# Kernel tuning notes

Measured on AMD Instinct MI355X. Metric: run time of the kernel, lower is better.

Reference implementation:

```python
import jax, jax.numpy as jnp
import numpy as np

B, D, H, L = 131072, 64, 256, 8  # batch, input_dim, hidden_dim, n_coupling_layers


def _alternating_masks():
    m = np.zeros((L, D), np.float32)
    m[:, ::2] = 1.0            # even layers: mask = 1,0,1,0,...
    m[1::2] = 1.0 - m[1::2]    # odd layers:  mask = 0,1,0,1,...
    return jnp.asarray(m)


def setup_inputs() -> dict:
    key = jax.random.key(0)
    ks = jax.random.split(key, 14)

    def lin_w(k, o, i):
        return (jax.random.normal(k, (L, o, i), jnp.float32) / np.sqrt(i))

    return {
        "x": jax.random.normal(ks[0], (B, D), jnp.float32),
        "masks": _alternating_masks(),                      # [L, D]
        # scale network params (stacked over layers)
        "sW1": lin_w(ks[1], H, D), "sb1": jnp.zeros((L, H), jnp.float32),
        "sW2": lin_w(ks[2], H, H), "sb2": jnp.zeros((L, H), jnp.float32),
        "sW3": lin_w(ks[3], D, H), "sb3": jnp.zeros((L, D), jnp.float32),
        "scale": 0.1 * jax.random.normal(ks[4], (L, D), jnp.float32),
        # translation network params
        "tW1": lin_w(ks[5], H, D), "tb1": jnp.zeros((L, H), jnp.float32),
        "tW2": lin_w(ks[6], H, H), "tb2": jnp.zeros((L, H), jnp.float32),
        "tW3": lin_w(ks[7], D, H), "tb3": jnp.zeros((L, D), jnp.float32),
    }


def _flow(x, masks, sW1, sb1, sW2, sb2, sW3, sb3, scale,
          tW1, tb1, tW2, tb2, tW3, tb3):
    def layer(carry, p):
        y, ld = carry
        m, W1, b1, W2, b2, W3, b3, sc, V1, c1, V2, c2, V3, c3 = p
        xm = y * m                                   # masked input [B, D]
        # scale net: residual tanh MLP, ends with +xm then elementwise *sc
        s = jnp.tanh(xm @ W1.T + b1)
        s = jnp.tanh(s @ W2.T + b2 + s)
        s = (jnp.tanh(s @ W3.T + b3) + xm) * sc
        # translation net
        t = jnp.tanh(xm @ V1.T + c1)
        t = jnp.tanh(t @ V2.T + c2 + t)
        t = (t @ V3.T + c3) + xm
        y2 = m * y + (1.0 - m) * (y * jnp.exp(s) + t)
        ld2 = ld + jnp.sum((1.0 - m) * s, -1)
        return (y2, ld2), None

    init = (x, jnp.zeros(x.shape[0], x.dtype))
    xs = (masks, sW1, sb1, sW2, sb2, sW3, sb3, scale,
          tW1, tb1, tW2, tb2, tW3, tb3)
    (y, logdet), _ = jax.lax.scan(layer, init, xs)
    return y, logdet


def reference(x, masks, sW1, sb1, sW2, sb2, sW3, sb3, scale,
              tW1, tb1, tW2, tb2, tW3, tb3):
    return _flow(x, masks, sW1, sb1, sW2, sb2, sW3, sb3, scale,
                 tW1, tb1, tW2, tb2, tW3, tb3)
```

## Files before the change

### kernel.cpp

```cpp
#include <hip/hip_runtime.h>


#define BATCH    131072
#define DIM      64
#define HID      256
#define NLAYER   8
#define BM       64
#define NTHREADS 256

#define ACT_S 264
#define XM_S  72
#define S3_S  68

typedef _Float16 f16;
typedef __attribute__((ext_vector_type(8))) _Float16 f16x8;
typedef __attribute__((ext_vector_type(4))) _Float16 f16x4;
typedef __attribute__((ext_vector_type(2))) _Float16 f16x2;
typedef __attribute__((ext_vector_type(4))) float    f32x4;

#define TWO_LOG2E 2.8853900817779268f
#define LOG2E     1.4426950408889634f

__device__ __forceinline__ float tanh_fast(float x) {
  float e = __builtin_amdgcn_exp2f(x * TWO_LOG2E);
  return 1.f - 2.f * __builtin_amdgcn_rcpf(e + 1.f);
}

__device__ __forceinline__ f16x4 pk4(float a, float b, float c, float d) {
  f16x2 lo = __builtin_bit_cast(f16x2, __builtin_amdgcn_cvt_pkrtz(a, b));
  f16x2 hi = __builtin_bit_cast(f16x2, __builtin_amdgcn_cvt_pkrtz(c, d));
  f16x4 o; o[0] = lo[0]; o[1] = lo[1]; o[2] = hi[0]; o[3] = hi[1];
  return o;
}

__global__ void cvt6_kernel(const float* s0, f16* d0, const float* s1, f16* d1,
                            const float* s2, f16* d2, const float* s3, f16* d3,
                            const float* s4, f16* d4, const float* s5, f16* d5) {
  int i = blockIdx.x * blockDim.x + threadIdx.x;
  const float* s; f16* d; int base;
  if      (i < 32768)  { s = s0; d = d0; base = 0; }
  else if (i < 163840) { s = s1; d = d1; base = 32768; }
  else if (i < 196608) { s = s2; d = d2; base = 163840; }
  else if (i < 229376) { s = s3; d = d3; base = 196608; }
  else if (i < 360448) { s = s4; d = d4; base = 229376; }
  else                 { s = s5; d = d5; base = 360448; }
  int k = i - base;
  float4 v = ((const float4*)s)[k];
  ((f16x4*)d)[k] = pk4(v.x, v.y, v.z, v.w);
}

__global__ __launch_bounds__(NTHREADS, 3) void flow_kernel(
    const float* __restrict__ x, const float* __restrict__ masks,
    const f16* __restrict__ wS1, const f16* __restrict__ wS2, const f16* __restrict__ wS3,
    const float* __restrict__ sb1, const float* __restrict__ sb2, const float* __restrict__ sb3,
    const float* __restrict__ scl,
    const f16* __restrict__ wT1, const f16* __restrict__ wT2, const f16* __restrict__ wT3,
    const float* __restrict__ tb1, const float* __restrict__ tb2, const float* __restrict__ tb3,
    float* __restrict__ y_out, float* __restrict__ ld_out)
{
  __shared__ __attribute__((aligned(16))) f16 act [BM * ACT_S];
  __shared__ __attribute__((aligned(16))) f16 xm_s[BM * XM_S];
  __shared__ __attribute__((aligned(16))) f16 s3_s[BM * S3_S];
  float* ld_red = (float*)xm_s;
  (void)masks;

  const int tid  = threadIdx.x;
  const int lane = tid & 63;
  const int wv   = tid >> 6;
  const int quad = lane >> 4;
  const int l16  = lane & 15;
  const int row0 = blockIdx.x * BM;
  const int d0   = wv * 16 + quad * 4;

  float yv[4][4];
  float lda[4];
  #pragma unroll
  for (int n = 0; n < 4; ++n) {
    const float4 v = *(const float4*)&x[(size_t)(row0 + n * 16 + l16) * DIM + d0];
    yv[n][0] = v.x; yv[n][1] = v.y; yv[n][2] = v.z; yv[n][3] = v.w;
    lda[n] = 0.f;
  }

  const f32x4 fzero = {0.f, 0.f, 0.f, 0.f};

  #pragma unroll 1
  for (int l = 0; l < NLAYER; ++l) {
    const int par = l & 1;

    if (par == 0) {
      #pragma unroll
      for (int n = 0; n < 4; ++n)
        *(f16x4*)&xm_s[(n * 16 + l16) * XM_S + d0] =
            pk4(yv[n][0], 0.f, yv[n][2], 0.f);
    } else {
      #pragma unroll
      for (int n = 0; n < 4; ++n)
        *(f16x4*)&xm_s[(n * 16 + l16) * XM_S + d0] =
            pk4(0.f, yv[n][1], 0.f, yv[n][3]);
    }
    __syncthreads();

    #pragma unroll 1
    for (int net = 0; net < 2; ++net) {
      const f16*   W1 = (net ? wT1 : wS1) + l * HID * DIM;
      const f16*   W2 = (net ? wT2 : wS2) + l * HID * HID;
      const f16*   W3 = (net ? wT3 : wS3) + l * DIM * HID;
      const float* b1 = (net ? tb1 : sb1) + l * HID;
      const float* b2 = (net ? tb2 : sb2) + l * HID;
      const float* b3 = (net ? tb3 : sb3) + l * DIM;

      f32x4 acc[4][4];
      #pragma unroll
      for (int m = 0; m < 4; ++m)
        #pragma unroll
        for (int n = 0; n < 4; ++n) acc[m][n] = fzero;

      #pragma unroll
      for (int kt = 0; kt < 2; ++kt) {
        const int k0 = kt * 32 + quad * 8;
        f16x8 afr[4];
        #pragma unroll
        for (int m = 0; m < 4; ++m)
          afr[m] = *(const f16x8*)&W1[(wv * 64 + m * 16 + l16) * DIM + k0];
        #pragma unroll
        for (int n = 0; n < 4; ++n) {
          const f16x8 bfr = *(const f16x8*)&xm_s[(n * 16 + l16) * XM_S + k0];
          #pragma unroll
          for (int m = 0; m < 4; ++m)
            acc[m][n] = __builtin_amdgcn_mfma_f32_16x16x32_f16(afr[m], bfr, acc[m][n], 0, 0, 0);
        }
      }
      #pragma unroll
      for (int m = 0; m < 4; ++m) {
        const int   h0  = wv * 64 + m * 16 + quad * 4;
        const float4 bv = *(const float4*)&b1[h0];
        #pragma unroll
        for (int n = 0; n < 4; ++n)
          *(f16x4*)&act[(n * 16 + l16) * ACT_S + h0] =
              pk4(tanh_fast(acc[m][n][0] + bv.x), tanh_fast(acc[m][n][1] + bv.y),
                  tanh_fast(acc[m][n][2] + bv.z), tanh_fast(acc[m][n][3] + bv.w));
      }
      __syncthreads();

      #pragma unroll
      for (int m = 0; m < 4; ++m)
        #pragma unroll
        for (int n = 0; n < 4; ++n) acc[m][n] = fzero;
      #pragma unroll 2
      for (int kt = 0; kt < 8; ++kt) {
        const int k0 = kt * 32 + quad * 8;
        f16x8 afr[4];
        #pragma unroll
        for (int m = 0; m < 4; ++m)
          afr[m] = *(const f16x8*)&W2[(wv * 64 + m * 16 + l16) * HID + k0];
        #pragma unroll
        for (int n = 0; n < 4; ++n) {
          const f16x8 bfr = *(const f16x8*)&act[(n * 16 + l16) * ACT_S + k0];
          #pragma unroll
          for (int m = 0; m < 4; ++m)
            acc[m][n] = __builtin_amdgcn_mfma_f32_16x16x32_f16(afr[m], bfr, acc[m][n], 0, 0, 0);
        }
      }
      __syncthreads();
      #pragma unroll
      for (int m = 0; m < 4; ++m) {
        const int   h0  = wv * 64 + m * 16 + quad * 4;
        const float4 bv = *(const float4*)&b2[h0];
        #pragma unroll
        for (int n = 0; n < 4; ++n) {
          f16x4* p = (f16x4*)&act[(n * 16 + l16) * ACT_S + h0];
          const f16x4 prev = *p;
          *p = pk4(tanh_fast(acc[m][n][0] + bv.x + (float)prev[0]),
                   tanh_fast(acc[m][n][1] + bv.y + (float)prev[1]),
                   tanh_fast(acc[m][n][2] + bv.z + (float)prev[2]),
                   tanh_fast(acc[m][n][3] + bv.w + (float)prev[3]));
        }
      }
      __syncthreads();

      f32x4 acc3[4];
      #pragma unroll
      for (int n = 0; n < 4; ++n) acc3[n] = fzero;
      #pragma unroll 2
      for (int kt = 0; kt < 8; ++kt) {
        const int k0  = kt * 32 + quad * 8;
        const f16x8 a3 = *(const f16x8*)&W3[(wv * 16 + l16) * HID + k0];
        #pragma unroll
        for (int n = 0; n < 4; ++n) {
          const f16x8 bfr = *(const f16x8*)&act[(n * 16 + l16) * ACT_S + k0];
          acc3[n] = __builtin_amdgcn_mfma_f32_16x16x32_f16(a3, bfr, acc3[n], 0, 0, 0);
        }
      }
      if (net == 0) __syncthreads();

      const float4 b3v = *(const float4*)&b3[d0];
      if (net == 0) {
        const float4 sv = *(const float4*)&scl[l * DIM + d0];
        if (par == 0) {
          #pragma unroll
          for (int n = 0; n < 4; ++n)
            *(f16x4*)&s3_s[(n * 16 + l16) * S3_S + d0] =
                pk4(0.f, tanh_fast(acc3[n][1] + b3v.y) * sv.y,
                    0.f, tanh_fast(acc3[n][3] + b3v.w) * sv.w);
        } else {
          #pragma unroll
          for (int n = 0; n < 4; ++n)
            *(f16x4*)&s3_s[(n * 16 + l16) * S3_S + d0] =
                pk4(tanh_fast(acc3[n][0] + b3v.x) * sv.x, 0.f,
                    tanh_fast(acc3[n][2] + b3v.z) * sv.z, 0.f);
        }
      } else {
        #define EP3I(n, r, BC) {                                         \
          const float s = (float)sh[r];                                  \
          const float e = __builtin_amdgcn_exp2f(s * LOG2E);             \
          yv[n][r] = yv[n][r] * e + (acc3[n][r] + (BC));                 \
          lda[n] += s; }
        if (par == 0) {
          #pragma unroll
          for (int n = 0; n < 4; ++n) {
            const f16x4 sh = *(const f16x4*)&s3_s[(n * 16 + l16) * S3_S + d0];
            EP3I(n, 1, b3v.y)
            EP3I(n, 3, b3v.w)
          }
        } else {
          #pragma unroll
          for (int n = 0; n < 4; ++n) {
            const f16x4 sh = *(const f16x4*)&s3_s[(n * 16 + l16) * S3_S + d0];
            EP3I(n, 0, b3v.x)
            EP3I(n, 2, b3v.z)
          }
        }
        #undef EP3I
      }
    }
  }

  #pragma unroll
  for (int n = 0; n < 4; ++n) {
    float4 v; v.x = yv[n][0]; v.y = yv[n][1]; v.z = yv[n][2]; v.w = yv[n][3];
    *(float4*)&y_out[(size_t)(row0 + n * 16 + l16) * DIM + d0] = v;
  }

  float v0 = lda[0], v1 = lda[1], v2 = lda[2], v3 = lda[3];
  v0 += __shfl_xor(v0, 16); v0 += __shfl_xor(v0, 32);
  v1 += __shfl_xor(v1, 16); v1 += __shfl_xor(v1, 32);
  v2 += __shfl_xor(v2, 16); v2 += __shfl_xor(v2, 32);
  v3 += __shfl_xor(v3, 16); v3 += __shfl_xor(v3, 32);
  __syncthreads();
  if (quad == 0) {
    ld_red[(0 * 16 + l16) * 4 + wv] = v0;
    ld_red[(1 * 16 + l16) * 4 + wv] = v1;
    ld_red[(2 * 16 + l16) * 4 + wv] = v2;
    ld_red[(3 * 16 + l16) * 4 + wv] = v3;
  }
  __syncthreads();
  if (tid < BM)
    ld_out[row0 + tid] = ld_red[tid * 4 + 0] + ld_red[tid * 4 + 1]
                       + ld_red[tid * 4 + 2] + ld_red[tid * 4 + 3];
}

extern "C" void kernel_launch(void* const* d_in, const int* in_sizes, int n_in,
                              void* d_out, int out_size, void* d_ws, size_t ws_size,
                              hipStream_t stream) {
  const float* x     = (const float*)d_in[0];
  const float* masks = (const float*)d_in[1];
  const float* sW1f  = (const float*)d_in[2];
  const float* sb1   = (const float*)d_in[3];
  const float* sW2f  = (const float*)d_in[4];
  const float* sb2   = (const float*)d_in[5];
  const float* sW3f  = (const float*)d_in[6];
  const float* sb3   = (const float*)d_in[7];
  const float* scl   = (const float*)d_in[8];
  const float* tW1f  = (const float*)d_in[9];
  const float* tb1   = (const float*)d_in[10];
  const float* tW2f  = (const float*)d_in[11];
  const float* tb2   = (const float*)d_in[12];
  const float* tW3f  = (const float*)d_in[13];
  const float* tb3   = (const float*)d_in[14];
  (void)in_sizes; (void)n_in; (void)out_size; (void)ws_size;

  const int W1SZ = NLAYER * HID * DIM;
  const int W2SZ = NLAYER * HID * HID;
  const int W3SZ = NLAYER * DIM * HID;
  f16* wS1 = (f16*)d_ws;
  f16* wS2 = wS1 + W1SZ;
  f16* wS3 = wS2 + W2SZ;
  f16* wT1 = wS3 + W3SZ;
  f16* wT2 = wT1 + W1SZ;
  f16* wT3 = wT2 + W2SZ;

  cvt6_kernel<<<1536, 256, 0, stream>>>(sW1f, wS1, sW2f, wS2, sW3f, wS3,
                                        tW1f, wT1, tW2f, wT2, tW3f, wT3);

  float* y_out  = (float*)d_out;
  float* ld_out = y_out + (size_t)BATCH * DIM;
  flow_kernel<<<BATCH / BM, NTHREADS, 0, stream>>>(
      x, masks, wS1, wS2, wS3, sb1, sb2, sb3, scl,
      wT1, wT2, wT3, tb1, tb2, tb3, y_out, ld_out);
}
```

Before: 896.7 us.

## Pack masked W1 columns, fold biases into accumulators, keep scale in registers

```diff
diff --git a/kernel.cpp b/kernel.cpp
--- a/kernel.cpp
+++ b/kernel.cpp
@@ -8,9 +8,8 @@
 #define BM       64
 #define NTHREADS 256
 
-#define ACT_S 264
-#define XM_S  72
-#define S3_S  68
+#define ACT_S  264
+#define XMP_S  32
 
 typedef _Float16 f16;
 typedef __attribute__((ext_vector_type(8))) _Float16 f16x8;
@@ -26,42 +25,58 @@
   return 1.f - 2.f * __builtin_amdgcn_rcpf(e + 1.f);
 }
 
+__device__ __forceinline__ f16x2 pk2(float a, float b) {
+  return __builtin_bit_cast(f16x2, __builtin_amdgcn_cvt_pkrtz(a, b));
+}
+
 __device__ __forceinline__ f16x4 pk4(float a, float b, float c, float d) {
-  f16x2 lo = __builtin_bit_cast(f16x2, __builtin_amdgcn_cvt_pkrtz(a, b));
-  f16x2 hi = __builtin_bit_cast(f16x2, __builtin_amdgcn_cvt_pkrtz(c, d));
+  f16x2 lo = pk2(a, b);
+  f16x2 hi = pk2(c, d);
   f16x4 o; o[0] = lo[0]; o[1] = lo[1]; o[2] = hi[0]; o[3] = hi[1];
   return o;
 }
 
-__global__ void cvt6_kernel(const float* s0, f16* d0, const float* s1, f16* d1,
-                            const float* s2, f16* d2, const float* s3, f16* d3,
-                            const float* s4, f16* d4, const float* s5, f16* d5) {
+__global__ void cvt4_kernel(const float* s0, f16* d0, const float* s1, f16* d1,
+                            const float* s2, f16* d2, const float* s3, f16* d3) {
   int i = blockIdx.x * blockDim.x + threadIdx.x;
   const float* s; f16* d; int base;
-  if      (i < 32768)  { s = s0; d = d0; base = 0; }
-  else if (i < 163840) { s = s1; d = d1; base = 32768; }
-  else if (i < 196608) { s = s2; d = d2; base = 163840; }
-  else if (i < 229376) { s = s3; d = d3; base = 196608; }
-  else if (i < 360448) { s = s4; d = d4; base = 229376; }
-  else                 { s = s5; d = d5; base = 360448; }
+  if      (i < 131072) { s = s0; d = d0; base = 0; }
+  else if (i < 163840) { s = s1; d = d1; base = 131072; }
+  else if (i < 294912) { s = s2; d = d2; base = 163840; }
+  else                 { s = s3; d = d3; base = 294912; }
   int k = i - base;
   float4 v = ((const float4*)s)[k];
   ((f16x4*)d)[k] = pk4(v.x, v.y, v.z, v.w);
 }
 
-__global__ __launch_bounds__(NTHREADS, 3) void flow_kernel(
+__global__ void cvtW1p_kernel(const float* sW1f, f16* dS,
+                              const float* tW1f, f16* dT) {
+  int i = blockIdx.x * blockDim.x + threadIdx.x;
+  const float* s = (i < 32768) ? sW1f : tW1f;
+  f16*         d = (i < 32768) ? dS   : dT;
+  int j   = i & 32767;
+  int l   = j >> 12;
+  int rem = j & 4095;
+  int h   = rem >> 4;
+  int kq  = rem & 15;
+  int par = l & 1;
+  const float a = s[l * 16384 + h * 64 + 4 * kq + par];
+  const float b = s[l * 16384 + h * 64 + 4 * kq + 2 + par];
+  ((f16x2*)d)[j] = pk2(a, b);
+}
+
+__global__ __launch_bounds__(NTHREADS, 4) void flow_kernel(
     const float* __restrict__ x, const float* __restrict__ masks,
-    const f16* __restrict__ wS1, const f16* __restrict__ wS2, const f16* __restrict__ wS3,
+    const f16* __restrict__ wS1p, const f16* __restrict__ wS2, const f16* __restrict__ wS3,
     const float* __restrict__ sb1, const float* __restrict__ sb2, const float* __restrict__ sb3,
     const float* __restrict__ scl,
-    const f16* __restrict__ wT1, const f16* __restrict__ wT2, const f16* __restrict__ wT3,
+    const f16* __restrict__ wT1p, const f16* __restrict__ wT2, const f16* __restrict__ wT3,
     const float* __restrict__ tb1, const float* __restrict__ tb2, const float* __restrict__ tb3,
     float* __restrict__ y_out, float* __restrict__ ld_out)
 {
   __shared__ __attribute__((aligned(16))) f16 act [BM * ACT_S];
-  __shared__ __attribute__((aligned(16))) f16 xm_s[BM * XM_S];
-  __shared__ __attribute__((aligned(16))) f16 s3_s[BM * S3_S];
-  float* ld_red = (float*)xm_s;
+  __shared__ __attribute__((aligned(16))) f16 xm_p[BM * XMP_S];
+  float* ld_red = (float*)xm_p;
   (void)masks;
 
   const int tid  = threadIdx.x;
@@ -71,8 +86,10 @@
   const int l16  = lane & 15;
   const int row0 = blockIdx.x * BM;
   const int d0   = wv * 16 + quad * 4;
-
-  float yv[4][4];
+  const int dp   = d0 >> 1;
+
+  float yv [4][4];
+  float s3r[4][2];
   float lda[4];
   #pragma unroll
   for (int n = 0; n < 4; ++n) {
@@ -81,8 +98,6 @@
     lda[n] = 0.f;
   }
 
-  const f32x4 fzero = {0.f, 0.f, 0.f, 0.f};
-
   #pragma unroll 1
   for (int l = 0; l < NLAYER; ++l) {
     const int par = l & 1;
@@ -90,41 +105,40 @@
     if (par == 0) {
       #pragma unroll
       for (int n = 0; n < 4; ++n)
-        *(f16x4*)&xm_s[(n * 16 + l16) * XM_S + d0] =
-            pk4(yv[n][0], 0.f, yv[n][2], 0.f);
+        *(f16x2*)&xm_p[(n * 16 + l16) * XMP_S + dp] = pk2(yv[n][0], yv[n][2]);
     } else {
       #pragma unroll
       for (int n = 0; n < 4; ++n)
-        *(f16x4*)&xm_s[(n * 16 + l16) * XM_S + d0] =
-            pk4(0.f, yv[n][1], 0.f, yv[n][3]);
+        *(f16x2*)&xm_p[(n * 16 + l16) * XMP_S + dp] = pk2(yv[n][1], yv[n][3]);
     }
     __syncthreads();
 
     #pragma unroll 1
     for (int net = 0; net < 2; ++net) {
-      const f16*   W1 = (net ? wT1 : wS1) + l * HID * DIM;
-      const f16*   W2 = (net ? wT2 : wS2) + l * HID * HID;
-      const f16*   W3 = (net ? wT3 : wS3) + l * DIM * HID;
+      const f16*   W1 = (net ? wT1p : wS1p) + l * HID * 32;
+      const f16*   W2 = (net ? wT2  : wS2)  + l * HID * HID;
+      const f16*   W3 = (net ? wT3  : wS3)  + l * DIM * HID;
       const float* b1 = (net ? tb1 : sb1) + l * HID;
       const float* b2 = (net ? tb2 : sb2) + l * HID;
       const float* b3 = (net ? tb3 : sb3) + l * DIM;
 
       f32x4 acc[4][4];
-      #pragma unroll
-      for (int m = 0; m < 4; ++m)
-        #pragma unroll
-        for (int n = 0; n < 4; ++n) acc[m][n] = fzero;
-
-      #pragma unroll
-      for (int kt = 0; kt < 2; ++kt) {
-        const int k0 = kt * 32 + quad * 8;
+
+      #pragma unroll
+      for (int m = 0; m < 4; ++m) {
+        const float4 bv = *(const float4*)&b1[wv * 64 + m * 16 + quad * 4];
+        f32x4 bi; bi[0] = bv.x; bi[1] = bv.y; bi[2] = bv.z; bi[3] = bv.w;
+        #pragma unroll
+        for (int n = 0; n < 4; ++n) acc[m][n] = bi;
+      }
+      {
         f16x8 afr[4];
         #pragma unroll
         for (int m = 0; m < 4; ++m)
-          afr[m] = *(const f16x8*)&W1[(wv * 64 + m * 16 + l16) * DIM + k0];
+          afr[m] = *(const f16x8*)&W1[(wv * 64 + m * 16 + l16) * 32 + quad * 8];
         #pragma unroll
         for (int n = 0; n < 4; ++n) {
-          const f16x8 bfr = *(const f16x8*)&xm_s[(n * 16 + l16) * XM_S + k0];
+          const f16x8 bfr = *(const f16x8*)&xm_p[(n * 16 + l16) * XMP_S + quad * 8];
           #pragma unroll
           for (int m = 0; m < 4; ++m)
             acc[m][n] = __builtin_amdgcn_mfma_f32_16x16x32_f16(afr[m], bfr, acc[m][n], 0, 0, 0);
@@ -132,20 +146,22 @@
       }
       #pragma unroll
       for (int m = 0; m < 4; ++m) {
-        const int   h0  = wv * 64 + m * 16 + quad * 4;
-        const float4 bv = *(const float4*)&b1[h0];
+        const int h0 = wv * 64 + m * 16 + quad * 4;
         #pragma unroll
         for (int n = 0; n < 4; ++n)
           *(f16x4*)&act[(n * 16 + l16) * ACT_S + h0] =
-              pk4(tanh_fast(acc[m][n][0] + bv.x), tanh_fast(acc[m][n][1] + bv.y),
-                  tanh_fast(acc[m][n][2] + bv.z), tanh_fast(acc[m][n][3] + bv.w));
+              pk4(tanh_fast(acc[m][n][0]), tanh_fast(acc[m][n][1]),
+                  tanh_fast(acc[m][n][2]), tanh_fast(acc[m][n][3]));
       }
       __syncthreads();
 
       #pragma unroll
-      for (int m = 0; m < 4; ++m)
-        #pragma unroll
-        for (int n = 0; n < 4; ++n) acc[m][n] = fzero;
+      for (int m = 0; m < 4; ++m) {
+        const float4 bv = *(const float4*)&b2[wv * 64 + m * 16 + quad * 4];
+        f32x4 bi; bi[0] = bv.x; bi[1] = bv.y; bi[2] = bv.z; bi[3] = bv.w;
+        #pragma unroll
+        for (int n = 0; n < 4; ++n) acc[m][n] = bi;
+      }
       #pragma unroll 2
       for (int kt = 0; kt < 8; ++kt) {
         const int k0 = kt * 32 + quad * 8;
@@ -164,23 +180,26 @@
       __syncthreads();
       #pragma unroll
       for (int m = 0; m < 4; ++m) {
-        const int   h0  = wv * 64 + m * 16 + quad * 4;
-        const float4 bv = *(const float4*)&b2[h0];
+        const int h0 = wv * 64 + m * 16 + quad * 4;
         #pragma unroll
         for (int n = 0; n < 4; ++n) {
           f16x4* p = (f16x4*)&act[(n * 16 + l16) * ACT_S + h0];
           const f16x4 prev = *p;
-          *p = pk4(tanh_fast(acc[m][n][0] + bv.x + (float)prev[0]),
-                   tanh_fast(acc[m][n][1] + bv.y + (float)prev[1]),
-                   tanh_fast(acc[m][n][2] + bv.z + (float)prev[2]),
-                   tanh_fast(acc[m][n][3] + bv.w + (float)prev[3]));
+          *p = pk4(tanh_fast(acc[m][n][0] + (float)prev[0]),
+                   tanh_fast(acc[m][n][1] + (float)prev[1]),
+                   tanh_fast(acc[m][n][2] + (float)prev[2]),
+                   tanh_fast(acc[m][n][3] + (float)prev[3]));
         }
       }
       __syncthreads();
 
       f32x4 acc3[4];
-      #pragma unroll
-      for (int n = 0; n < 4; ++n) acc3[n] = fzero;
+      {
+        const float4 bv = *(const float4*)&b3[d0];
+        f32x4 bi; bi[0] = bv.x; bi[1] = bv.y; bi[2] = bv.z; bi[3] = bv.w;
+        #pragma unroll
+        for (int n = 0; n < 4; ++n) acc3[n] = bi;
+      }
       #pragma unroll 2
       for (int kt = 0; kt < 8; ++kt) {
         const int k0  = kt * 32 + quad * 8;
@@ -193,41 +212,38 @@
       }
       if (net == 0) __syncthreads();
 
-      const float4 b3v = *(const float4*)&b3[d0];
       if (net == 0) {
         const float4 sv = *(const float4*)&scl[l * DIM + d0];
         if (par == 0) {
           #pragma unroll
-          for (int n = 0; n < 4; ++n)
-            *(f16x4*)&s3_s[(n * 16 + l16) * S3_S + d0] =
-                pk4(0.f, tanh_fast(acc3[n][1] + b3v.y) * sv.y,
-                    0.f, tanh_fast(acc3[n][3] + b3v.w) * sv.w);
+          for (int n = 0; n < 4; ++n) {
+            s3r[n][0] = tanh_fast(acc3[n][1]) * sv.y;
+            s3r[n][1] = tanh_fast(acc3[n][3]) * sv.w;
+          }
         } else {
           #pragma unroll
-          for (int n = 0; n < 4; ++n)
-            *(f16x4*)&s3_s[(n * 16 + l16) * S3_S + d0] =
-                pk4(tanh_fast(acc3[n][0] + b3v.x) * sv.x, 0.f,
-                    tanh_fast(acc3[n][2] + b3v.z) * sv.z, 0.f);
+          for (int n = 0; n < 4; ++n) {
+            s3r[n][0] = tanh_fast(acc3[n][0]) * sv.x;
+            s3r[n][1] = tanh_fast(acc3[n][2]) * sv.z;
+          }
         }
       } else {
-        #define EP3I(n, r, BC) {                                         \
-          const float s = (float)sh[r];                                  \
+        #define EP3I(n, r, SS) {                                         \
+          const float s = (SS);                                          \
           const float e = __builtin_amdgcn_exp2f(s * LOG2E);             \
-          yv[n][r] = yv[n][r] * e + (acc3[n][r] + (BC));                 \
+          yv[n][r] = yv[n][r] * e + acc3[n][r];                          \
           lda[n] += s; }
         if (par == 0) {
           #pragma unroll
           for (int n = 0; n < 4; ++n) {
-            const f16x4 sh = *(const f16x4*)&s3_s[(n * 16 + l16) * S3_S + d0];
-            EP3I(n, 1, b3v.y)
-            EP3I(n, 3, b3v.w)
+            EP3I(n, 1, s3r[n][0])
+            EP3I(n, 3, s3r[n][1])
           }
         } else {
           #pragma unroll
           for (int n = 0; n < 4; ++n) {
-            const f16x4 sh = *(const f16x4*)&s3_s[(n * 16 + l16) * S3_S + d0];
-            EP3I(n, 0, b3v.x)
-            EP3I(n, 2, b3v.z)
+            EP3I(n, 0, s3r[n][0])
+            EP3I(n, 2, s3r[n][1])
           }
         }
         #undef EP3I
@@ -279,22 +295,22 @@
   const float* tb3   = (const float*)d_in[14];
   (void)in_sizes; (void)n_in; (void)out_size; (void)ws_size;
 
-  const int W1SZ = NLAYER * HID * DIM;
-  const int W2SZ = NLAYER * HID * HID;
-  const int W3SZ = NLAYER * DIM * HID;
-  f16* wS1 = (f16*)d_ws;
-  f16* wS2 = wS1 + W1SZ;
-  f16* wS3 = wS2 + W2SZ;
-  f16* wT1 = wS3 + W3SZ;
-  f16* wT2 = wT1 + W1SZ;
-  f16* wT3 = wT2 + W2SZ;
-
-  cvt6_kernel<<<1536, 256, 0, stream>>>(sW1f, wS1, sW2f, wS2, sW3f, wS3,
-                                        tW1f, wT1, tW2f, wT2, tW3f, wT3);
+  const int W1PSZ = NLAYER * HID * 32;
+  const int W2SZ  = NLAYER * HID * HID;
+  const int W3SZ  = NLAYER * DIM * HID;
+  f16* wS1p = (f16*)d_ws;
+  f16* wS2  = wS1p + W1PSZ;
+  f16* wS3  = wS2 + W2SZ;
+  f16* wT1p = wS3 + W3SZ;
+  f16* wT2  = wT1p + W1PSZ;
+  f16* wT3  = wT2 + W2SZ;
+
+  cvt4_kernel<<<1280, 256, 0, stream>>>(sW2f, wS2, sW3f, wS3, tW2f, wT2, tW3f, wT3);
+  cvtW1p_kernel<<<256, 256, 0, stream>>>(sW1f, wS1p, tW1f, wT1p);
 
   float* y_out  = (float*)d_out;
   float* ld_out = y_out + (size_t)BATCH * DIM;
   flow_kernel<<<BATCH / BM, NTHREADS, 0, stream>>>(
-      x, masks, wS1, wS2, wS3, sb1, sb2, sb3, scl,
-      wT1, wT2, wT3, tb1, tb2, tb3, y_out, ld_out);
-}
+      x, masks, wS1p, wS2, wS3, sb1, sb2, sb3, scl,
+      wT1p, wT2, wT3, tb1, tb2, tb3, y_out, ld_out);
+}
```

New measurement: 983.7 us. 1.1x slower.
